# Kernel optimization log

Hardware: AMD Instinct MI355X
Metric: run time of the kernel (lower is better)

The kernel has to match this reference:

```python
import jax, jax.numpy as jnp
import numpy as np

N_FILTER = 64
IMAGE_SIZE = 64
CHANNELS = 3
N_CALLS = 16  # n_calls * 16 with n_calls=1
EPS = 1e-5


def _sobel_kernels(c):
    kx = jnp.array([[-1., 0., 1.], [-2., 0., 2.], [-1., 0., 1.]], jnp.float32) / 8.0
    ky = kx.T
    # depthwise OIHW kernels: (C, 1, 3, 3)
    return jnp.tile(kx[None, None], (c, 1, 1, 1)), jnp.tile(ky[None, None], (c, 1, 1, 1))


def _dwconv(x, k):
    return jax.lax.conv_general_dilated(
        x, k, window_strides=(1, 1), padding='SAME',
        feature_group_count=x.shape[1],
        dimension_numbers=('NCHW', 'OIHW', 'NCHW'))


def setup_inputs() -> dict:
    key = jax.random.key(0)
    k1, k2, k3 = jax.random.split(key, 3)
    B, L = 16, 512
    fin, fout = N_FILTER * 3, N_FILTER
    return {
        'lat': jax.random.normal(k1, (B, L), jnp.float32),
        'Wk': jax.random.normal(k2, (L, fin * fout), jnp.float32) * 0.02,
        'bk': jnp.zeros((fin * fout,), jnp.float32),
        'Wb': jax.random.normal(k3, (L, fout), jnp.float32) * 0.02,
        'bb': jnp.zeros((fout,), jnp.float32),
        'leak_factor': jnp.asarray(0.1, jnp.float32),
    }


def reference(lat, Wk, bk, Wb, bb, leak_factor):
    B = lat.shape[0]
    fin, fout = N_FILTER * 3, N_FILTER
    kx, ky = _sobel_kernels(N_FILTER)

    # seed: zeros with a 1.0 in channel 0 at the image center
    out0 = jnp.zeros((B, N_FILTER, IMAGE_SIZE, IMAGE_SIZE), jnp.float32)
    out0 = out0.at[:, 0, IMAGE_SIZE // 2, IMAGE_SIZE // 2].set(1.0)

    leak = jnp.clip(leak_factor, 0.001, 1000.0)

    # per-sample dynamic 1x1 conv weights/bias (constant across the loop)
    w = (lat @ Wk + bk).reshape(B, fout, fin)   # (B, fout, fin)
    b = (lat @ Wb + bb)                          # (B, fout)

    def step(out, _):
        # Sobel perception: [identity, grad_x, grad_y] -> (B, 3*nf, H, W)
        p = jnp.concatenate([out, _dwconv(out, kx), _dwconv(out, ky)], axis=1)
        # InstanceNorm2d (affine=False): normalize over H, W per sample/channel
        mu = p.mean(axis=(2, 3), keepdims=True)
        var = p.var(axis=(2, 3), keepdims=True)
        p = (p - mu) * jax.lax.rsqrt(var + EPS)
        # latent-conditioned dynamic 1x1 conv
        new = jnp.einsum('bchw,boc->bohw', p, w) + b[:, :, None, None]
        out = out + leak * new
        return out, out

    out, embs = jax.lax.scan(step, out0, None, length=N_CALLS)
    out_embs = jnp.concatenate([out0[None], embs], axis=0)  # (N_CALLS+1, B, nf, H, W)

    out_raw = out[:, :CHANNELS]
    return jnp.clip(out_raw, -1.0, 1.0), out_embs, out_raw
```

## Files before the change

kernel.cpp:

```cpp
#include <hip/hip_runtime.h>
#include <cstdint>
#include <cstddef>

#define NB 16
#define NC 64
#define HW 4096
#define SLICE ((size_t)(NB*NC*HW))
#define NSTEP 16

#define WS_WT    ((size_t)0)
#define WS_BV    ((size_t)196608)
#define WS_LATT  ((size_t)197632)
#define WS_SV    ((size_t)205824)
#define WS_SVMU  ((size_t)208896)

typedef _Float16 half8 __attribute__((ext_vector_type(8)));
typedef float f32x4 __attribute__((ext_vector_type(4)));

__global__ void k_latT(const float* __restrict__ lat, float* __restrict__ latT) {
  int t = threadIdx.x;
  for (int idx = t; idx < 16*512; idx += 256) {
    int b = idx >> 9, k = idx & 511;
    latT[k*16 + b] = lat[idx];
  }
}

__global__ __launch_bounds__(256) void k_w(const float* __restrict__ latT,
    const float* __restrict__ Wk, const float* __restrict__ bk,
    const float* __restrict__ Wb, const float* __restrict__ bb,
    float* __restrict__ wT, float* __restrict__ bvec) {
  int t = threadIdx.x;
  if (blockIdx.x < 48) {
    int j = blockIdx.x*256 + t;
    float acc[16];
#pragma unroll
    for (int b = 0; b < 16; b++) acc[b] = 0.f;
#pragma unroll 4
    for (int k = 0; k < 512; k++) {
      float wv = Wk[(size_t)k*12288 + j];
      const float* lt = (const float*)__builtin_assume_aligned(latT + k*16, 64);
#pragma unroll
      for (int b = 0; b < 16; b++) acc[b] = fmaf(lt[b], wv, acc[b]);
    }
    int o = j / 192, cf = j % 192;
    int g = cf >> 6, c = cf & 63;
    float bkj = bk[j];
#pragma unroll
    for (int b = 0; b < 16; b++)
      wT[(((size_t)(b*3 + g))*64 + o)*64 + c] = acc[b] + bkj;
  } else if (t < 64) {
    int j = t;
    float acc[16];
#pragma unroll
    for (int b = 0; b < 16; b++) acc[b] = 0.f;
    for (int k = 0; k < 512; k++) {
      float wv = Wb[k*64 + j];
      const float* lt = (const float*)__builtin_assume_aligned(latT + k*16, 64);
#pragma unroll
      for (int b = 0; b < 16; b++) acc[b] = fmaf(lt[b], wv, acc[b]);
    }
    float bbj = bb[j];
#pragma unroll
    for (int b = 0; b < 16; b++) bvec[b*64 + j] = acc[b] + bbj;
  }
}

__global__ void k_init(float* __restrict__ e0) {
  int idx4 = (blockIdx.x*256 + threadIdx.x) * 4;
  float4 v = make_float4(0.f, 0.f, 0.f, 0.f);
  if ((idx4 & 262143) == 2080) v.x = 1.0f;
  *(float4*)(e0 + idx4) = v;
}

__global__ __launch_bounds__(256) void k_stats(const float* __restrict__ st,
    float* __restrict__ svb, float* __restrict__ svmub) {
  int c = blockIdx.x, b = blockIdx.y, t = threadIdx.x;
  __shared__ float img[HW];
  __shared__ float red[4][6];
  const size_t chan = (size_t)(b*NC + c) * HW;
  const float4* src4 = (const float4*)(st + chan);
  float4* img4 = (float4*)img;
#pragma unroll
  for (int i = 0; i < 4; i++) img4[i*256 + t] = src4[i*256 + t];
  __syncthreads();
  float s0=0,q0=0,s1=0,q1=0,s2=0,q2=0;
#pragma unroll
  for (int i = 0; i < 4; i++) {
    int base = i*1024 + t*4;
    int h = base >> 6, w0 = base & 63;
#pragma unroll
    for (int jj = 0; jj < 4; jj++) {
      int w = w0 + jj;
      bool wl = (w > 0), wr = (w < 63), hu = (h > 0), hd = (h < 63);
      float a00 = (hu && wl) ? img[(h-1)*64 + (w-1)] : 0.f;
      float a01 =  hu        ? img[(h-1)*64 +  w   ] : 0.f;
      float a02 = (hu && wr) ? img[(h-1)*64 + (w+1)] : 0.f;
      float a10 =  wl        ? img[ h   *64 + (w-1)] : 0.f;
      float a12 =  wr        ? img[ h   *64 + (w+1)] : 0.f;
      float a20 = (hd && wl) ? img[(h+1)*64 + (w-1)] : 0.f;
      float a21 =  hd        ? img[(h+1)*64 +  w   ] : 0.f;
      float a22 = (hd && wr) ? img[(h+1)*64 + (w+1)] : 0.f;
      float v = img[h*64 + w];
      float gx = (a02 - a00 + 2.f*(a12 - a10) + a22 - a20) * 0.125f;
      float gy = (a20 - a00 + 2.f*(a21 - a01) + a22 - a02) * 0.125f;
      s0 += v;  q0 = fmaf(v, v, q0);
      s1 += gx; q1 = fmaf(gx, gx, q1);
      s2 += gy; q2 = fmaf(gy, gy, q2);
    }
  }
#pragma unroll
  for (int off = 32; off >= 1; off >>= 1) {
    s0 += __shfl_xor(s0, off); q0 += __shfl_xor(q0, off);
    s1 += __shfl_xor(s1, off); q1 += __shfl_xor(q1, off);
    s2 += __shfl_xor(s2, off); q2 += __shfl_xor(q2, off);
  }
  int lane = t & 63, wv = t >> 6;
  if (lane == 0) {
    red[wv][0]=s0; red[wv][1]=q0; red[wv][2]=s1;
    red[wv][3]=q1; red[wv][4]=s2; red[wv][5]=q2;
  }
  __syncthreads();
  if (t == 0) {
    float r[6];
#pragma unroll
    for (int u = 0; u < 6; u++) r[u] = red[0][u]+red[1][u]+red[2][u]+red[3][u];
#pragma unroll
    for (int g = 0; g < 3; g++) {
      float mu  = r[2*g] * (1.f/HW);
      float var = fmaxf(r[2*g+1]*(1.f/HW) - mu*mu, 0.f);
      float sv  = 1.f / sqrtf(var + 1e-5f);
      svb  [b*192 + g*64 + c] = sv;
      svmub[b*192 + g*64 + c] = sv * mu;
    }
  }
}

__global__ __launch_bounds__(256, 2) void k_fused(const float* __restrict__ st,
    float* __restrict__ stn, const float* __restrict__ wT,
    const float* __restrict__ bvec, const float* __restrict__ svb,
    const float* __restrict__ svmub, const float* __restrict__ leakp) {
  int r = blockIdx.x, b = blockIdx.y, t = threadIdx.x;
  __shared__ __align__(16) float rawL[32*200];
  __shared__ __align__(16) _Float16 Bhi[4*192*8];
  __shared__ __align__(16) _Float16 Blo[4*192*8];
  __shared__ __align__(16) _Float16 Whi[3*64*32];
  __shared__ __align__(16) _Float16 Wlo[3*64*32];
  __shared__ float svL[192], svmuL[192], biasL[192], bvecL[64];

  if (t < 192) { svL[t] = svb[b*192 + t]; svmuL[t] = svmub[b*192 + t]; }
  if (t < 64) bvecL[t] = bvec[b*64 + t];
  float leak = fminf(fmaxf(leakp[0], 0.001f), 1000.f);

  int lane = t & 63;
  int wt = t >> 6;
  const float* stb = st + (size_t)b*NC*HW;
  float biasacc = 0.f;
  f32x4 accA[4] = {}; f32x4 accB[12] = {}; f32x4 accC[12] = {};

  for (int kc = 0; kc < 2; kc++) {
    __syncthreads();
#pragma unroll
    for (int i = 0; i < 6; i++) {
      int u = t + i*256;
      int c_rel = u / 48, q = u % 48;
      int rho = q >> 4, quad = q & 15;
      int row = r - 1 + rho;
      float4 v = make_float4(0.f,0.f,0.f,0.f);
      if (row >= 0 && row < 64)
        v = *(const float4*)(stb + (size_t)(kc*32 + c_rel)*HW + row*64 + quad*4);
      *(float4*)(rawL + c_rel*200 + rho*64 + quad*4) = v;
    }
    if (t < 192) {
      int g = t >> 6, o = t & 63;
      const float* wrow = wT + (((size_t)(b*3 + g))*64 + o)*64 + kc*32;
#pragma unroll
      for (int s = 0; s < 4; s++) {
        float4 va = *(const float4*)(wrow + s*8);
        float4 vb = *(const float4*)(wrow + s*8 + 4);
        float wv[8] = {va.x,va.y,va.z,va.w,vb.x,vb.y,vb.z,vb.w};
        half8 hv, lv;
#pragma unroll
        for (int jj = 0; jj < 8; jj++) {
          int cg = g*64 + kc*32 + s*8 + jj;
          float scaled = wv[jj] * svL[cg];
          biasacc = fmaf(wv[jj], svmuL[cg], biasacc);
          _Float16 h = (_Float16)scaled;
          hv[jj] = h;
          lv[jj] = (_Float16)(scaled - (float)h);
        }
        int sidx = (g*64 + o)*32 + ((s ^ (o & 3)) << 3);
        *(half8*)(Whi + sidx) = hv;
        *(half8*)(Wlo + sidx) = lv;
      }
    }
    __syncthreads();
#pragma unroll
    for (int i = 0; i < 3; i++) {
      int v = t + i*256;
      int c8 = v / 192, px = v % 192;
      half8 hv, lv;
#pragma unroll
      for (int ii = 0; ii < 8; ii++) {
        float x = rawL[(c8*8 + ii)*200 + px];
        _Float16 h = (_Float16)x;
        hv[ii] = h;
        lv[ii] = (_Float16)(x - (float)h);
      }
      *(half8*)(Bhi + (c8*192 + px)*8) = hv;
      *(half8*)(Blo + (c8*192 + px)*8) = lv;
    }
    __syncthreads();
    half8 ahi[3], alo[3];
#pragma unroll
    for (int g = 0; g < 3; g++) {
      int oa = wt*16 + (lane & 15);
      int sidx = (g*64 + oa)*32 + (((lane >> 4) ^ (oa & 3)) << 3);
      ahi[g] = *(const half8*)(Whi + sidx);
      alo[g] = *(const half8*)(Wlo + sidx);
    }
#pragma unroll
    for (int n = 0; n < 12; n++) {
      int bidx = ((lane >> 4)*192 + n*16 + (lane & 15))*8;
      half8 bh = *(const half8*)(Bhi + bidx);
      half8 bl = *(const half8*)(Blo + bidx);
      accB[n] = __builtin_amdgcn_mfma_f32_16x16x32_f16(ahi[1], bh, accB[n], 0,0,0);
      accB[n] = __builtin_amdgcn_mfma_f32_16x16x32_f16(ahi[1], bl, accB[n], 0,0,0);
      accB[n] = __builtin_amdgcn_mfma_f32_16x16x32_f16(alo[1], bh, accB[n], 0,0,0);
      accC[n] = __builtin_amdgcn_mfma_f32_16x16x32_f16(ahi[2], bh, accC[n], 0,0,0);
      accC[n] = __builtin_amdgcn_mfma_f32_16x16x32_f16(ahi[2], bl, accC[n], 0,0,0);
      accC[n] = __builtin_amdgcn_mfma_f32_16x16x32_f16(alo[2], bh, accC[n], 0,0,0);
      if (n >= 4 && n < 8) {
        accA[n-4] = __builtin_amdgcn_mfma_f32_16x16x32_f16(ahi[0], bh, accA[n-4], 0,0,0);
        accA[n-4] = __builtin_amdgcn_mfma_f32_16x16x32_f16(ahi[0], bl, accA[n-4], 0,0,0);
        accA[n-4] = __builtin_amdgcn_mfma_f32_16x16x32_f16(alo[0], bh, accA[n-4], 0,0,0);
      }
    }
  }

  if (t < 192) biasL[t] = biasacc;
  __syncthreads();

#pragma unroll
  for (int j = 0; j < 4; j++) {
    int o = wt*16 + ((lane >> 4) << 2) + j;
    float Sx[4], Sy[4];
#pragma unroll
    for (int nc = 0; nc < 4; nc++) {
      Sx[nc] = accB[nc][j] + 2.f*accB[4+nc][j] + accB[8+nc][j];
      Sy[nc] = accC[8+nc][j] - accC[nc][j];
    }
    float bt = bvecL[o] - biasL[o] - biasL[64+o] - biasL[128+o];
#pragma unroll
    for (int nc = 0; nc < 4; nc++) {
      int nm = (nc > 0) ? nc-1 : 0;
      int np = (nc < 3) ? nc+1 : 3;
      float xl1 = __shfl(Sx[nc], (lane - 1) & 63);
      float xl2 = (nc > 0) ? __shfl(Sx[nm], (lane + 15) & 63) : 0.f;
      float xL  = (lane & 15) ? xl1 : xl2;
      float xr1 = __shfl(Sx[nc], (lane + 1) & 63);
      float xr2 = (nc < 3) ? __shfl(Sx[np], (lane - 15) & 63) : 0.f;
      float xR  = ((lane & 15) == 15) ? xr2 : xr1;
      float yl1 = __shfl(Sy[nc], (lane - 1) & 63);
      float yl2 = (nc > 0) ? __shfl(Sy[nm], (lane + 15) & 63) : 0.f;
      float yL  = (lane & 15) ? yl1 : yl2;
      float yr1 = __shfl(Sy[nc], (lane + 1) & 63);
      float yr2 = (nc < 3) ? __shfl(Sy[np], (lane - 15) & 63) : 0.f;
      float yR  = ((lane & 15) == 15) ? yr2 : yr1;
      float gx = (xR - xL) * 0.125f;
      float gy = (yL + 2.f*Sy[nc] + yR) * 0.125f;
      float nw = accA[nc][j] + gx + gy + bt;
      int w = nc*16 + (lane & 15);
      size_t gi = (size_t)(b*NC + o)*HW + (size_t)r*64 + w;
      stn[gi] = st[gi] + leak * nw;
    }
  }
}

__global__ void k_final(const float* __restrict__ stF, float* __restrict__ out0,
                        float* __restrict__ out2) {
  int i4 = (blockIdx.x*256 + threadIdx.x)*4;
  int b = i4 / 12288, rr = i4 % 12288;
  float4 v = *(const float4*)(stF + (size_t)b*(NC*HW) + rr);
  float4 cv;
  cv.x = fminf(fmaxf(v.x,-1.f),1.f);
  cv.y = fminf(fmaxf(v.y,-1.f),1.f);
  cv.z = fminf(fmaxf(v.z,-1.f),1.f);
  cv.w = fminf(fmaxf(v.w,-1.f),1.f);
  *(float4*)(out0 + i4) = cv;
  *(float4*)(out2 + i4) = v;
}

extern "C" void kernel_launch(void* const* d_in, const int* in_sizes, int n_in,
                              void* d_out, int out_size, void* d_ws, size_t ws_size,
                              hipStream_t stream) {
  const float* lat   = (const float*)d_in[0];
  const float* Wk    = (const float*)d_in[1];
  const float* bk    = (const float*)d_in[2];
  const float* Wb    = (const float*)d_in[3];
  const float* bb    = (const float*)d_in[4];
  const float* leakp = (const float*)d_in[5];
  float* out = (float*)d_out;
  float* ws  = (float*)d_ws;
  float* wT    = ws + WS_WT;
  float* bvec  = ws + WS_BV;
  float* latT  = ws + WS_LATT;
  float* svbuf = ws + WS_SV;
  float* svmub = ws + WS_SVMU;
  float* out0 = out;
  float* embs = out + 196608;
  float* out2 = out + 196608 + 17*SLICE;

  hipLaunchKernelGGL(k_latT, dim3(1),    dim3(256), 0, stream, lat, latT);
  hipLaunchKernelGGL(k_w,    dim3(49),   dim3(256), 0, stream, latT, Wk, bk, Wb, bb, wT, bvec);
  hipLaunchKernelGGL(k_init, dim3(4096), dim3(256), 0, stream, embs);
  for (int tstep = 0; tstep < NSTEP; tstep++) {
    const float* stc = embs + (size_t)tstep*SLICE;
    float*       stn = embs + (size_t)(tstep+1)*SLICE;
    hipLaunchKernelGGL(k_stats, dim3(64,16), dim3(256), 0, stream, stc, svbuf, svmub);
    hipLaunchKernelGGL(k_fused, dim3(64,16), dim3(256), 0, stream,
                       stc, stn, wT, bvec, svbuf, svmub, leakp);
  }
  hipLaunchKernelGGL(k_final, dim3(192), dim3(256), 0, stream,
                     embs + (size_t)NSTEP*SLICE, out0, out2);
}
```

Before: 730.2 us.

## Pipeline k_fused channel chunks, swizzle LDS, slide stats window, fold final kernel

```diff
diff --git a/kernel.cpp b/kernel.cpp
--- a/kernel.cpp
+++ b/kernel.cpp
@@ -83,30 +83,45 @@
 #pragma unroll
   for (int i = 0; i < 4; i++) img4[i*256 + t] = src4[i*256 + t];
   __syncthreads();
+
+  int w = t & 63;
+  int h0 = (t >> 6) * 16;
+  bool wl = (w > 0), wr = (w < 63);
   float s0=0,q0=0,s1=0,q1=0,s2=0,q2=0;
-#pragma unroll
-  for (int i = 0; i < 4; i++) {
-    int base = i*1024 + t*4;
-    int h = base >> 6, w0 = base & 63;
-#pragma unroll
-    for (int jj = 0; jj < 4; jj++) {
-      int w = w0 + jj;
-      bool wl = (w > 0), wr = (w < 63), hu = (h > 0), hd = (h < 63);
-      float a00 = (hu && wl) ? img[(h-1)*64 + (w-1)] : 0.f;
-      float a01 =  hu        ? img[(h-1)*64 +  w   ] : 0.f;
-      float a02 = (hu && wr) ? img[(h-1)*64 + (w+1)] : 0.f;
-      float a10 =  wl        ? img[ h   *64 + (w-1)] : 0.f;
-      float a12 =  wr        ? img[ h   *64 + (w+1)] : 0.f;
-      float a20 = (hd && wl) ? img[(h+1)*64 + (w-1)] : 0.f;
-      float a21 =  hd        ? img[(h+1)*64 +  w   ] : 0.f;
-      float a22 = (hd && wr) ? img[(h+1)*64 + (w+1)] : 0.f;
-      float v = img[h*64 + w];
-      float gx = (a02 - a00 + 2.f*(a12 - a10) + a22 - a20) * 0.125f;
-      float gy = (a20 - a00 + 2.f*(a21 - a01) + a22 - a02) * 0.125f;
-      s0 += v;  q0 = fmaf(v, v, q0);
-      s1 += gx; q1 = fmaf(gx, gx, q1);
-      s2 += gy; q2 = fmaf(gy, gy, q2);
-    }
+  float d_prev=0.f, s_prev=0.f, d_cur, s_cur, v_cur;
+  if (h0 > 0) {
+    const float* row = img + (h0-1)*64;
+    float xl = wl ? row[w-1] : 0.f;
+    float xc = row[w];
+    float xr = wr ? row[w+1] : 0.f;
+    d_prev = xr - xl; s_prev = xl + 2.f*xc + xr;
+  }
+  {
+    const float* row = img + h0*64;
+    float xl = wl ? row[w-1] : 0.f;
+    float xc = row[w];
+    float xr = wr ? row[w+1] : 0.f;
+    d_cur = xr - xl; s_cur = xl + 2.f*xc + xr; v_cur = xc;
+  }
+#pragma unroll
+  for (int k = 0; k < 16; k++) {
+    int hn = h0 + k + 1;
+    float d_nxt=0.f, s_nxt=0.f, v_nxt=0.f;
+    if (hn < 64) {
+      const float* row = img + hn*64;
+      float xl = wl ? row[w-1] : 0.f;
+      float xc = row[w];
+      float xr = wr ? row[w+1] : 0.f;
+      d_nxt = xr - xl; s_nxt = xl + 2.f*xc + xr; v_nxt = xc;
+    }
+    float gx = (d_prev + 2.f*d_cur + d_nxt) * 0.125f;
+    float gy = (s_nxt - s_prev) * 0.125f;
+    float v = v_cur;
+    s0 += v;  q0 = fmaf(v, v, q0);
+    s1 += gx; q1 = fmaf(gx, gx, q1);
+    s2 += gy; q2 = fmaf(gy, gy, q2);
+    d_prev = d_cur; s_prev = s_cur;
+    d_cur = d_nxt; s_cur = s_nxt; v_cur = v_nxt;
   }
 #pragma unroll
   for (int off = 32; off >= 1; off >>= 1) {
@@ -135,109 +150,141 @@
   }
 }
 
+struct SB {
+  alignas(16) _Float16 Bhi[6144];
+  alignas(16) _Float16 Blo[6144];
+  alignas(16) _Float16 Whi[6144];
+  alignas(16) _Float16 Wlo[6144];
+  float svL[192], svmuL[192], biasL[192], bvecL[64];
+};
+
 __global__ __launch_bounds__(256, 2) void k_fused(const float* __restrict__ st,
     float* __restrict__ stn, const float* __restrict__ wT,
     const float* __restrict__ bvec, const float* __restrict__ svb,
-    const float* __restrict__ svmub, const float* __restrict__ leakp) {
-  int r = blockIdx.x, b = blockIdx.y, t = threadIdx.x;
-  __shared__ __align__(16) float rawL[32*200];
-  __shared__ __align__(16) _Float16 Bhi[4*192*8];
-  __shared__ __align__(16) _Float16 Blo[4*192*8];
-  __shared__ __align__(16) _Float16 Whi[3*64*32];
-  __shared__ __align__(16) _Float16 Wlo[3*64*32];
-  __shared__ float svL[192], svmuL[192], biasL[192], bvecL[64];
-
-  if (t < 192) { svL[t] = svb[b*192 + t]; svmuL[t] = svmub[b*192 + t]; }
-  if (t < 64) bvecL[t] = bvec[b*64 + t];
+    const float* __restrict__ svmub, const float* __restrict__ leakp,
+    float* __restrict__ out0, float* __restrict__ out2, int last) {
+  __shared__ SB sh;
+  int bid = blockIdx.x, t = threadIdx.x;
+  int b = bid >> 6;
+  int r = (bid & 7) * 8 + ((bid >> 3) & 7);
+  int lane = t & 63, wt = t >> 6;
+  const float* stb = st + (size_t)b*NC*HW;
   float leak = fminf(fmaxf(leakp[0], 0.001f), 1000.f);
 
-  int lane = t & 63;
-  int wt = t >> 6;
-  const float* stb = st + (size_t)b*NC*HW;
+  if (t < 192) { sh.svL[t] = svb[b*192 + t]; sh.svmuL[t] = svmub[b*192 + t]; }
+  if (t < 64) sh.bvecL[t] = bvec[b*64 + t];
+
   float biasacc = 0.f;
   f32x4 accA[4] = {}; f32x4 accB[12] = {}; f32x4 accC[12] = {};
-
-  for (int kc = 0; kc < 2; kc++) {
-    __syncthreads();
-#pragma unroll
-    for (int i = 0; i < 6; i++) {
-      int u = t + i*256;
-      int c_rel = u / 48, q = u % 48;
-      int rho = q >> 4, quad = q & 15;
-      int row = r - 1 + rho;
-      float4 v = make_float4(0.f,0.f,0.f,0.f);
-      if (row >= 0 && row < 64)
-        v = *(const float4*)(stb + (size_t)(kc*32 + c_rel)*HW + row*64 + quad*4);
-      *(float4*)(rawL + c_rel*200 + rho*64 + quad*4) = v;
-    }
-    if (t < 192) {
-      int g = t >> 6, o = t & 63;
-      const float* wrow = wT + (((size_t)(b*3 + g))*64 + o)*64 + kc*32;
-#pragma unroll
-      for (int s = 0; s < 4; s++) {
-        float4 va = *(const float4*)(wrow + s*8);
-        float4 vb = *(const float4*)(wrow + s*8 + 4);
-        float wv[8] = {va.x,va.y,va.z,va.w,vb.x,vb.y,vb.z,vb.w};
-        half8 hv, lv;
-#pragma unroll
-        for (int jj = 0; jj < 8; jj++) {
-          int cg = g*64 + kc*32 + s*8 + jj;
-          float scaled = wv[jj] * svL[cg];
-          biasacc = fmaf(wv[jj], svmuL[cg], biasacc);
-          _Float16 h = (_Float16)scaled;
-          hv[jj] = h;
-          lv[jj] = (_Float16)(scaled - (float)h);
-        }
-        int sidx = (g*64 + o)*32 + ((s ^ (o & 3)) << 3);
-        *(half8*)(Whi + sidx) = hv;
-        *(half8*)(Wlo + sidx) = lv;
-      }
-    }
-    __syncthreads();
-#pragma unroll
-    for (int i = 0; i < 3; i++) {
-      int v = t + i*256;
-      int c8 = v / 192, px = v % 192;
-      half8 hv, lv;
-#pragma unroll
-      for (int ii = 0; ii < 8; ii++) {
-        float x = rawL[(c8*8 + ii)*200 + px];
-        _Float16 h = (_Float16)x;
-        hv[ii] = h;
-        lv[ii] = (_Float16)(x - (float)h);
-      }
-      *(half8*)(Bhi + (c8*192 + px)*8) = hv;
-      *(half8*)(Blo + (c8*192 + px)*8) = lv;
-    }
-    __syncthreads();
-    half8 ahi[3], alo[3];
-#pragma unroll
-    for (int g = 0; g < 3; g++) {
-      int oa = wt*16 + (lane & 15);
-      int sidx = (g*64 + oa)*32 + (((lane >> 4) ^ (oa & 3)) << 3);
-      ahi[g] = *(const half8*)(Whi + sidx);
-      alo[g] = *(const half8*)(Wlo + sidx);
-    }
-#pragma unroll
-    for (int n = 0; n < 12; n++) {
-      int bidx = ((lane >> 4)*192 + n*16 + (lane & 15))*8;
-      half8 bh = *(const half8*)(Bhi + bidx);
-      half8 bl = *(const half8*)(Blo + bidx);
-      accB[n] = __builtin_amdgcn_mfma_f32_16x16x32_f16(ahi[1], bh, accB[n], 0,0,0);
-      accB[n] = __builtin_amdgcn_mfma_f32_16x16x32_f16(ahi[1], bl, accB[n], 0,0,0);
-      accB[n] = __builtin_amdgcn_mfma_f32_16x16x32_f16(alo[1], bh, accB[n], 0,0,0);
-      accC[n] = __builtin_amdgcn_mfma_f32_16x16x32_f16(ahi[2], bh, accC[n], 0,0,0);
-      accC[n] = __builtin_amdgcn_mfma_f32_16x16x32_f16(ahi[2], bl, accC[n], 0,0,0);
-      accC[n] = __builtin_amdgcn_mfma_f32_16x16x32_f16(alo[2], bh, accC[n], 0,0,0);
-      if (n >= 4 && n < 8) {
-        accA[n-4] = __builtin_amdgcn_mfma_f32_16x16x32_f16(ahi[0], bh, accA[n-4], 0,0,0);
-        accA[n-4] = __builtin_amdgcn_mfma_f32_16x16x32_f16(ahi[0], bl, accA[n-4], 0,0,0);
-        accA[n-4] = __builtin_amdgcn_mfma_f32_16x16x32_f16(alo[0], bh, accA[n-4], 0,0,0);
-      }
-    }
-  }
-
-  if (t < 192) biasL[t] = biasacc;
+  float xw0[3][8], xw1[3][8];
+
+#define LOADW(KC, XW)                                                    \
+  _Pragma("unroll")                                                      \
+  for (int i = 0; i < 3; i++) {                                          \
+    int u = t + i*256;                                                   \
+    int c8 = u / 192, pxu = u % 192;                                     \
+    int rho = pxu >> 6, ww = pxu & 63;                                   \
+    int row = r - 1 + rho;                                               \
+    bool ok = (row >= 0) && (row < 64);                                  \
+    int rowc = ok ? row : 0;                                             \
+    const float* gp = stb + (size_t)((KC)*32 + c8*8)*HW + rowc*64 + ww;  \
+    _Pragma("unroll")                                                    \
+    for (int ii = 0; ii < 8; ii++) {                                     \
+      float val = gp[(size_t)ii*HW];                                     \
+      XW[i][ii] = ok ? val : 0.f;                                        \
+    }                                                                    \
+  }
+
+#define PACKW(XW)                                                        \
+  _Pragma("unroll")                                                      \
+  for (int i = 0; i < 3; i++) {                                          \
+    int u = t + i*256;                                                   \
+    int c8 = u / 192, pxu = u % 192;                                     \
+    half8 hv, lv;                                                        \
+    _Pragma("unroll")                                                    \
+    for (int ii = 0; ii < 8; ii++) {                                     \
+      float x = XW[i][ii];                                               \
+      _Float16 h = (_Float16)x;                                          \
+      hv[ii] = h;                                                        \
+      lv[ii] = (_Float16)(x - (float)h);                                 \
+    }                                                                    \
+    int di = (c8*192 + (pxu ^ c8)) * 8;                                  \
+    *(half8*)(sh.Bhi + di) = hv;                                         \
+    *(half8*)(sh.Blo + di) = lv;                                         \
+  }
+
+#define WSTAGE(KC)                                                       \
+  if (t < 192) {                                                         \
+    int g = t >> 6, o = t & 63;                                          \
+    const float* wrow = wT + (((size_t)(b*3 + g))*64 + o)*64 + (KC)*32;  \
+    _Pragma("unroll")                                                    \
+    for (int s = 0; s < 4; s++) {                                        \
+      float4 va = *(const float4*)(wrow + s*8);                          \
+      float4 vb4 = *(const float4*)(wrow + s*8 + 4);                     \
+      float wv[8] = {va.x,va.y,va.z,va.w,vb4.x,vb4.y,vb4.z,vb4.w};       \
+      half8 hv, lv;                                                      \
+      _Pragma("unroll")                                                  \
+      for (int jj = 0; jj < 8; jj++) {                                   \
+        int cg = g*64 + (KC)*32 + s*8 + jj;                              \
+        float scaled = wv[jj] * sh.svL[cg];                              \
+        biasacc = fmaf(wv[jj], sh.svmuL[cg], biasacc);                   \
+        _Float16 h = (_Float16)scaled;                                   \
+        hv[jj] = h;                                                      \
+        lv[jj] = (_Float16)(scaled - (float)h);                          \
+      }                                                                  \
+      int swz = (s ^ (o & 3) ^ ((o >> 2) & 3)) & 3;                      \
+      int sidx = (g*64 + o)*32 + (swz << 3);                             \
+      *(half8*)(sh.Whi + sidx) = hv;                                     \
+      *(half8*)(sh.Wlo + sidx) = lv;                                     \
+    }                                                                    \
+  }
+
+#define MFMAS()                                                          \
+  {                                                                      \
+    half8 ahi[3], alo[3];                                                \
+    int oa = wt*16 + (lane & 15);                                        \
+    int c4 = lane >> 4;                                                  \
+    int slotx = (c4 ^ (oa & 3) ^ ((oa >> 2) & 3)) & 3;                   \
+    _Pragma("unroll")                                                    \
+    for (int g = 0; g < 3; g++) {                                        \
+      int sidx = (g*64 + oa)*32 + (slotx << 3);                          \
+      ahi[g] = *(const half8*)(sh.Whi + sidx);                           \
+      alo[g] = *(const half8*)(sh.Wlo + sidx);                           \
+    }                                                                    \
+    _Pragma("unroll")                                                    \
+    for (int n = 0; n < 12; n++) {                                       \
+      int px = n*16 + (lane & 15);                                       \
+      int bidx = (c4*192 + (px ^ c4))*8;                                 \
+      half8 bh = *(const half8*)(sh.Bhi + bidx);                         \
+      half8 bl = *(const half8*)(sh.Blo + bidx);                         \
+      accB[n] = __builtin_amdgcn_mfma_f32_16x16x32_f16(ahi[1], bh, accB[n], 0,0,0); \
+      accB[n] = __builtin_amdgcn_mfma_f32_16x16x32_f16(ahi[1], bl, accB[n], 0,0,0); \
+      accB[n] = __builtin_amdgcn_mfma_f32_16x16x32_f16(alo[1], bh, accB[n], 0,0,0); \
+      accC[n] = __builtin_amdgcn_mfma_f32_16x16x32_f16(ahi[2], bh, accC[n], 0,0,0); \
+      accC[n] = __builtin_amdgcn_mfma_f32_16x16x32_f16(ahi[2], bl, accC[n], 0,0,0); \
+      accC[n] = __builtin_amdgcn_mfma_f32_16x16x32_f16(alo[2], bh, accC[n], 0,0,0); \
+      if (n >= 4 && n < 8) {                                             \
+        accA[n-4] = __builtin_amdgcn_mfma_f32_16x16x32_f16(ahi[0], bh, accA[n-4], 0,0,0); \
+        accA[n-4] = __builtin_amdgcn_mfma_f32_16x16x32_f16(ahi[0], bl, accA[n-4], 0,0,0); \
+        accA[n-4] = __builtin_amdgcn_mfma_f32_16x16x32_f16(alo[0], bh, accA[n-4], 0,0,0); \
+      }                                                                  \
+    }                                                                    \
+  }
+
+  LOADW(0, xw0)
+  __syncthreads();
+  PACKW(xw0)
+  WSTAGE(0)
+  __syncthreads();
+  LOADW(1, xw1)
+  MFMAS()
+  __syncthreads();
+  PACKW(xw1)
+  WSTAGE(1)
+  __syncthreads();
+  MFMAS()
+
+  if (t < 192) sh.biasL[t] = biasacc;
   __syncthreads();
 
 #pragma unroll
@@ -249,7 +296,7 @@
       Sx[nc] = accB[nc][j] + 2.f*accB[4+nc][j] + accB[8+nc][j];
       Sy[nc] = accC[8+nc][j] - accC[nc][j];
     }
-    float bt = bvecL[o] - biasL[o] - biasL[64+o] - biasL[128+o];
+    float bt = sh.bvecL[o] - sh.biasL[o] - sh.biasL[64+o] - sh.biasL[128+o];
 #pragma unroll
     for (int nc = 0; nc < 4; nc++) {
       int nm = (nc > 0) ? nc-1 : 0;
@@ -269,25 +316,21 @@
       float gx = (xR - xL) * 0.125f;
       float gy = (yL + 2.f*Sy[nc] + yR) * 0.125f;
       float nw = accA[nc][j] + gx + gy + bt;
-      int w = nc*16 + (lane & 15);
-      size_t gi = (size_t)(b*NC + o)*HW + (size_t)r*64 + w;
-      stn[gi] = st[gi] + leak * nw;
-    }
-  }
-}
-
-__global__ void k_final(const float* __restrict__ stF, float* __restrict__ out0,
-                        float* __restrict__ out2) {
-  int i4 = (blockIdx.x*256 + threadIdx.x)*4;
-  int b = i4 / 12288, rr = i4 % 12288;
-  float4 v = *(const float4*)(stF + (size_t)b*(NC*HW) + rr);
-  float4 cv;
-  cv.x = fminf(fmaxf(v.x,-1.f),1.f);
-  cv.y = fminf(fmaxf(v.y,-1.f),1.f);
-  cv.z = fminf(fmaxf(v.z,-1.f),1.f);
-  cv.w = fminf(fmaxf(v.w,-1.f),1.f);
-  *(float4*)(out0 + i4) = cv;
-  *(float4*)(out2 + i4) = v;
+      int wpx = nc*16 + (lane & 15);
+      size_t gi = (size_t)(b*NC + o)*HW + (size_t)r*64 + wpx;
+      float nv = st[gi] + leak * nw;
+      stn[gi] = nv;
+      if (last && o < 3) {
+        size_t oi = (size_t)(b*3 + o)*HW + (size_t)r*64 + wpx;
+        out2[oi] = nv;
+        out0[oi] = fminf(fmaxf(nv, -1.f), 1.f);
+      }
+    }
+  }
+#undef LOADW
+#undef PACKW
+#undef WSTAGE
+#undef MFMAS
 }
 
 extern "C" void kernel_launch(void* const* d_in, const int* in_sizes, int n_in,
@@ -317,9 +360,8 @@
     const float* stc = embs + (size_t)tstep*SLICE;
     float*       stn = embs + (size_t)(tstep+1)*SLICE;
     hipLaunchKernelGGL(k_stats, dim3(64,16), dim3(256), 0, stream, stc, svbuf, svmub);
-    hipLaunchKernelGGL(k_fused, dim3(64,16), dim3(256), 0, stream,
-                       stc, stn, wT, bvec, svbuf, svmub, leakp);
-  }
-  hipLaunchKernelGGL(k_final, dim3(192), dim3(256), 0, stream,
-                     embs + (size_t)NSTEP*SLICE, out0, out2);
-}
+    hipLaunchKernelGGL(k_fused, dim3(1024), dim3(256), 0, stream,
+                       stc, stn, wT, bvec, svbuf, svmub, leakp,
+                       out0, out2, (int)(tstep == NSTEP-1));
+  }
+}
```

New measurement: 599.9 us. 17.9% less time.

## Precompute fp16 hi/lo state planes, two rows per block, fuse final output

Applied to the files above, without the earlier changes.

```diff
diff --git a/kernel.cpp b/kernel.cpp
--- a/kernel.cpp
+++ b/kernel.cpp
@@ -10,22 +10,15 @@
 
 #define WS_WT    ((size_t)0)
 #define WS_BV    ((size_t)196608)
-#define WS_LATT  ((size_t)197632)
-#define WS_SV    ((size_t)205824)
-#define WS_SVMU  ((size_t)208896)
+#define WS_SV    ((size_t)197632)
+#define WS_SVMU  ((size_t)200704)
+#define WS_PLA   ((size_t)203776)
+#define WS_PLB   ((size_t)4398080)
 
 typedef _Float16 half8 __attribute__((ext_vector_type(8)));
 typedef float f32x4 __attribute__((ext_vector_type(4)));
 
-__global__ void k_latT(const float* __restrict__ lat, float* __restrict__ latT) {
-  int t = threadIdx.x;
-  for (int idx = t; idx < 16*512; idx += 256) {
-    int b = idx >> 9, k = idx & 511;
-    latT[k*16 + b] = lat[idx];
-  }
-}
-
-__global__ __launch_bounds__(256) void k_w(const float* __restrict__ latT,
+__global__ __launch_bounds__(256) void k_w(const float* __restrict__ lat,
     const float* __restrict__ Wk, const float* __restrict__ bk,
     const float* __restrict__ Wb, const float* __restrict__ bb,
     float* __restrict__ wT, float* __restrict__ bvec) {
@@ -38,9 +31,8 @@
 #pragma unroll 4
     for (int k = 0; k < 512; k++) {
       float wv = Wk[(size_t)k*12288 + j];
-      const float* lt = (const float*)__builtin_assume_aligned(latT + k*16, 64);
-#pragma unroll
-      for (int b = 0; b < 16; b++) acc[b] = fmaf(lt[b], wv, acc[b]);
+#pragma unroll
+      for (int b = 0; b < 16; b++) acc[b] = fmaf(lat[b*512 + k], wv, acc[b]);
     }
     int o = j / 192, cf = j % 192;
     int g = cf >> 6, c = cf & 63;
@@ -55,9 +47,8 @@
     for (int b = 0; b < 16; b++) acc[b] = 0.f;
     for (int k = 0; k < 512; k++) {
       float wv = Wb[k*64 + j];
-      const float* lt = (const float*)__builtin_assume_aligned(latT + k*16, 64);
-#pragma unroll
-      for (int b = 0; b < 16; b++) acc[b] = fmaf(lt[b], wv, acc[b]);
+#pragma unroll
+      for (int b = 0; b < 16; b++) acc[b] = fmaf(lat[b*512 + k], wv, acc[b]);
     }
     float bbj = bb[j];
 #pragma unroll
@@ -65,48 +56,50 @@
   }
 }
 
-__global__ void k_init(float* __restrict__ e0) {
-  int idx4 = (blockIdx.x*256 + threadIdx.x) * 4;
+__global__ void k_init(float* __restrict__ e0, float* __restrict__ plA) {
+  int f4 = blockIdx.x*256 + threadIdx.x;
   float4 v = make_float4(0.f, 0.f, 0.f, 0.f);
-  if ((idx4 & 262143) == 2080) v.x = 1.0f;
-  *(float4*)(e0 + idx4) = v;
+  if (f4 < 1048576) {
+    if ((f4 & 65535) == 520) v.x = 1.0f;
+    *(float4*)(e0 + (size_t)f4*4) = v;
+  } else {
+    int g4 = f4 - 1048576;
+    if ((g4 & 65535) == 2080)
+      v.x = __uint_as_float(0x00003C00u);
+    *(float4*)(plA + (size_t)g4*4) = v;
+  }
 }
 
 __global__ __launch_bounds__(256) void k_stats(const float* __restrict__ st,
     float* __restrict__ svb, float* __restrict__ svmub) {
   int c = blockIdx.x, b = blockIdx.y, t = threadIdx.x;
-  __shared__ float img[HW];
   __shared__ float red[4][6];
-  const size_t chan = (size_t)(b*NC + c) * HW;
-  const float4* src4 = (const float4*)(st + chan);
-  float4* img4 = (float4*)img;
-#pragma unroll
-  for (int i = 0; i < 4; i++) img4[i*256 + t] = src4[i*256 + t];
-  __syncthreads();
+  const float* base = st + (size_t)(b*NC + c) * HW;
+  int w = t & 63, wv = t >> 6, h0 = wv * 16;
+  float x[18];
+#pragma unroll
+  for (int i = 0; i < 18; i++) {
+    int row = h0 - 1 + i;
+    x[i] = (row >= 0 && row < 64) ? base[row*64 + w] : 0.f;
+  }
+  float d[18], s[18];
+#pragma unroll
+  for (int i = 0; i < 18; i++) {
+    float xl = __shfl(x[i], (w + 63) & 63);
+    float xr = __shfl(x[i], (w + 1) & 63);
+    if (w == 0)  xl = 0.f;
+    if (w == 63) xr = 0.f;
+    d[i] = xr - xl; s[i] = xl + 2.f*x[i] + xr;
+  }
   float s0=0,q0=0,s1=0,q1=0,s2=0,q2=0;
 #pragma unroll
-  for (int i = 0; i < 4; i++) {
-    int base = i*1024 + t*4;
-    int h = base >> 6, w0 = base & 63;
-#pragma unroll
-    for (int jj = 0; jj < 4; jj++) {
-      int w = w0 + jj;
-      bool wl = (w > 0), wr = (w < 63), hu = (h > 0), hd = (h < 63);
-      float a00 = (hu && wl) ? img[(h-1)*64 + (w-1)] : 0.f;
-      float a01 =  hu        ? img[(h-1)*64 +  w   ] : 0.f;
-      float a02 = (hu && wr) ? img[(h-1)*64 + (w+1)] : 0.f;
-      float a10 =  wl        ? img[ h   *64 + (w-1)] : 0.f;
-      float a12 =  wr        ? img[ h   *64 + (w+1)] : 0.f;
-      float a20 = (hd && wl) ? img[(h+1)*64 + (w-1)] : 0.f;
-      float a21 =  hd        ? img[(h+1)*64 +  w   ] : 0.f;
-      float a22 = (hd && wr) ? img[(h+1)*64 + (w+1)] : 0.f;
-      float v = img[h*64 + w];
-      float gx = (a02 - a00 + 2.f*(a12 - a10) + a22 - a20) * 0.125f;
-      float gy = (a20 - a00 + 2.f*(a21 - a01) + a22 - a02) * 0.125f;
-      s0 += v;  q0 = fmaf(v, v, q0);
-      s1 += gx; q1 = fmaf(gx, gx, q1);
-      s2 += gy; q2 = fmaf(gy, gy, q2);
-    }
+  for (int k = 0; k < 16; k++) {
+    float v  = x[k+1];
+    float gx = (d[k] + 2.f*d[k+1] + d[k+2]) * 0.125f;
+    float gy = (s[k+2] - s[k]) * 0.125f;
+    s0 += v;  q0 = fmaf(v, v, q0);
+    s1 += gx; q1 = fmaf(gx, gx, q1);
+    s2 += gy; q2 = fmaf(gy, gy, q2);
   }
 #pragma unroll
   for (int off = 32; off >= 1; off >>= 1) {
@@ -114,7 +107,7 @@
     s1 += __shfl_xor(s1, off); q1 += __shfl_xor(q1, off);
     s2 += __shfl_xor(s2, off); q2 += __shfl_xor(q2, off);
   }
-  int lane = t & 63, wv = t >> 6;
+  int lane = t & 63;
   if (lane == 0) {
     red[wv][0]=s0; red[wv][1]=q0; red[wv][2]=s1;
     red[wv][3]=q1; red[wv][4]=s2; red[wv][5]=q2;
@@ -135,159 +128,170 @@
   }
 }
 
-__global__ __launch_bounds__(256, 2) void k_fused(const float* __restrict__ st,
+struct SG {
+  alignas(16) _Float16 Bwin[32768];
+  float biasL[64];
+};
+
+__global__ __launch_bounds__(256, 2) void k_gemm(const float* __restrict__ st,
     float* __restrict__ stn, const float* __restrict__ wT,
     const float* __restrict__ bvec, const float* __restrict__ svb,
-    const float* __restrict__ svmub, const float* __restrict__ leakp) {
-  int r = blockIdx.x, b = blockIdx.y, t = threadIdx.x;
-  __shared__ __align__(16) float rawL[32*200];
-  __shared__ __align__(16) _Float16 Bhi[4*192*8];
-  __shared__ __align__(16) _Float16 Blo[4*192*8];
-  __shared__ __align__(16) _Float16 Whi[3*64*32];
-  __shared__ __align__(16) _Float16 Wlo[3*64*32];
-  __shared__ float svL[192], svmuL[192], biasL[192], bvecL[64];
-
-  if (t < 192) { svL[t] = svb[b*192 + t]; svmuL[t] = svmub[b*192 + t]; }
-  if (t < 64) bvecL[t] = bvec[b*64 + t];
+    const float* __restrict__ svmub, const _Float16* __restrict__ plR,
+    _Float16* __restrict__ plW, const float* __restrict__ leakp,
+    float* __restrict__ out0, float* __restrict__ out2, int last) {
+  __shared__ SG sh;
+  int bid = blockIdx.x, t = threadIdx.x;
+  int b = bid >> 5;
+  int r0 = ((((bid & 7) << 2) | ((bid >> 3) & 3))) << 1;
+  int lane = t & 63, wt = t >> 6, c4 = lane >> 4;
   float leak = fminf(fmaxf(leakp[0], 0.001f), 1000.f);
 
-  int lane = t & 63;
-  int wt = t >> 6;
-  const float* stb = st + (size_t)b*NC*HW;
+  const _Float16* plb = plR + (size_t)b*524288;
+#pragma unroll
+  for (int i = 0; i < 16; i++) {
+    int u = t + i*256;
+    int pl = u >> 11, rest = u & 2047;
+    int pxg = (r0 - 1)*64 + (rest & 255);
+    int pxc = pxg < 0 ? 0 : (pxg > 4095 ? 4095 : pxg);
+    const _Float16* gp = plb + ((size_t)pl*8 + (rest >> 8))*32768 + (size_t)pxc*8;
+    float4 v = *(const float4*)gp;
+    if (pxg < 0 || pxg > 4095) v = make_float4(0.f,0.f,0.f,0.f);
+    *(float4*)(sh.Bwin + (size_t)u*8) = v;
+  }
+
+  int oa = wt*16 + (lane & 15);
+  half8 whi[3][2], wlo[3][2];
   float biasacc = 0.f;
-  f32x4 accA[4] = {}; f32x4 accB[12] = {}; f32x4 accC[12] = {};
-
-  for (int kc = 0; kc < 2; kc++) {
-    __syncthreads();
-#pragma unroll
-    for (int i = 0; i < 6; i++) {
-      int u = t + i*256;
-      int c_rel = u / 48, q = u % 48;
-      int rho = q >> 4, quad = q & 15;
-      int row = r - 1 + rho;
-      float4 v = make_float4(0.f,0.f,0.f,0.f);
-      if (row >= 0 && row < 64)
-        v = *(const float4*)(stb + (size_t)(kc*32 + c_rel)*HW + row*64 + quad*4);
-      *(float4*)(rawL + c_rel*200 + rho*64 + quad*4) = v;
-    }
-    if (t < 192) {
-      int g = t >> 6, o = t & 63;
-      const float* wrow = wT + (((size_t)(b*3 + g))*64 + o)*64 + kc*32;
-#pragma unroll
-      for (int s = 0; s < 4; s++) {
-        float4 va = *(const float4*)(wrow + s*8);
-        float4 vb = *(const float4*)(wrow + s*8 + 4);
-        float wv[8] = {va.x,va.y,va.z,va.w,vb.x,vb.y,vb.z,vb.w};
-        half8 hv, lv;
-#pragma unroll
-        for (int jj = 0; jj < 8; jj++) {
-          int cg = g*64 + kc*32 + s*8 + jj;
-          float scaled = wv[jj] * svL[cg];
-          biasacc = fmaf(wv[jj], svmuL[cg], biasacc);
-          _Float16 h = (_Float16)scaled;
-          hv[jj] = h;
-          lv[jj] = (_Float16)(scaled - (float)h);
+#pragma unroll
+  for (int g = 0; g < 3; g++) {
+#pragma unroll
+    for (int kc = 0; kc < 2; kc++) {
+      const float* wrow = wT + (((size_t)(b*3 + g))*64 + oa)*64 + kc*32 + c4*8;
+      const float* svp  = svb   + b*192 + g*64 + kc*32 + c4*8;
+      const float* svmp = svmub + b*192 + g*64 + kc*32 + c4*8;
+      float4 wa = *(const float4*)wrow;  float4 wb2 = *(const float4*)(wrow + 4);
+      float4 sa = *(const float4*)svp;   float4 sb2 = *(const float4*)(svp + 4);
+      float4 ma = *(const float4*)svmp;  float4 mb2 = *(const float4*)(svmp + 4);
+      float wv[8] = {wa.x,wa.y,wa.z,wa.w, wb2.x,wb2.y,wb2.z,wb2.w};
+      float sv[8] = {sa.x,sa.y,sa.z,sa.w, sb2.x,sb2.y,sb2.z,sb2.w};
+      float mv[8] = {ma.x,ma.y,ma.z,ma.w, mb2.x,mb2.y,mb2.z,mb2.w};
+      half8 hv, lv;
+#pragma unroll
+      for (int jj = 0; jj < 8; jj++) {
+        float scaled = wv[jj] * sv[jj];
+        biasacc = fmaf(wv[jj], mv[jj], biasacc);
+        _Float16 h = (_Float16)scaled;
+        hv[jj] = h;
+        lv[jj] = (_Float16)(scaled - (float)h);
+      }
+      whi[g][kc] = hv; wlo[g][kc] = lv;
+    }
+  }
+  biasacc += __shfl_xor(biasacc, 16);
+  biasacc += __shfl_xor(biasacc, 32);
+  if (c4 == 0) sh.biasL[oa] = bvec[b*64 + oa] - biasacc;
+  __syncthreads();
+
+#pragma unroll
+  for (int rr = 0; rr < 2; rr++) {
+    int r = r0 + rr;
+    f32x4 accA[4] = {}; f32x4 accB[12] = {}; f32x4 accC[12] = {};
+#pragma unroll
+    for (int kc = 0; kc < 2; kc++) {
+#pragma unroll
+      for (int n = 0; n < 12; n++) {
+        int pxl = rr*64 + n*16 + (lane & 15);
+        half8 bh = *(const half8*)(sh.Bwin + ((size_t)(     kc*4 + c4)*256 + pxl)*8);
+        half8 bl = *(const half8*)(sh.Bwin + ((size_t)(8 +  kc*4 + c4)*256 + pxl)*8);
+        accB[n] = __builtin_amdgcn_mfma_f32_16x16x32_f16(whi[1][kc], bh, accB[n], 0,0,0);
+        accB[n] = __builtin_amdgcn_mfma_f32_16x16x32_f16(whi[1][kc], bl, accB[n], 0,0,0);
+        accB[n] = __builtin_amdgcn_mfma_f32_16x16x32_f16(wlo[1][kc], bh, accB[n], 0,0,0);
+        accC[n] = __builtin_amdgcn_mfma_f32_16x16x32_f16(whi[2][kc], bh, accC[n], 0,0,0);
+        accC[n] = __builtin_amdgcn_mfma_f32_16x16x32_f16(whi[2][kc], bl, accC[n], 0,0,0);
+        accC[n] = __builtin_amdgcn_mfma_f32_16x16x32_f16(wlo[2][kc], bh, accC[n], 0,0,0);
+        if (n >= 4 && n < 8) {
+          accA[n-4] = __builtin_amdgcn_mfma_f32_16x16x32_f16(whi[0][kc], bh, accA[n-4], 0,0,0);
+          accA[n-4] = __builtin_amdgcn_mfma_f32_16x16x32_f16(whi[0][kc], bl, accA[n-4], 0,0,0);
+          accA[n-4] = __builtin_amdgcn_mfma_f32_16x16x32_f16(wlo[0][kc], bh, accA[n-4], 0,0,0);
         }
-        int sidx = (g*64 + o)*32 + ((s ^ (o & 3)) << 3);
-        *(half8*)(Whi + sidx) = hv;
-        *(half8*)(Wlo + sidx) = lv;
-      }
-    }
-    __syncthreads();
-#pragma unroll
-    for (int i = 0; i < 3; i++) {
-      int v = t + i*256;
-      int c8 = v / 192, px = v % 192;
-      half8 hv, lv;
-#pragma unroll
-      for (int ii = 0; ii < 8; ii++) {
-        float x = rawL[(c8*8 + ii)*200 + px];
-        _Float16 h = (_Float16)x;
-        hv[ii] = h;
-        lv[ii] = (_Float16)(x - (float)h);
-      }
-      *(half8*)(Bhi + (c8*192 + px)*8) = hv;
-      *(half8*)(Blo + (c8*192 + px)*8) = lv;
-    }
-    __syncthreads();
-    half8 ahi[3], alo[3];
-#pragma unroll
-    for (int g = 0; g < 3; g++) {
-      int oa = wt*16 + (lane & 15);
-      int sidx = (g*64 + oa)*32 + (((lane >> 4) ^ (oa & 3)) << 3);
-      ahi[g] = *(const half8*)(Whi + sidx);
-      alo[g] = *(const half8*)(Wlo + sidx);
-    }
-#pragma unroll
-    for (int n = 0; n < 12; n++) {
-      int bidx = ((lane >> 4)*192 + n*16 + (lane & 15))*8;
-      half8 bh = *(const half8*)(Bhi + bidx);
-      half8 bl = *(const half8*)(Blo + bidx);
-      accB[n] = __builtin_amdgcn_mfma_f32_16x16x32_f16(ahi[1], bh, accB[n], 0,0,0);
-      accB[n] = __builtin_amdgcn_mfma_f32_16x16x32_f16(ahi[1], bl, accB[n], 0,0,0);
-      accB[n] = __builtin_amdgcn_mfma_f32_16x16x32_f16(alo[1], bh, accB[n], 0,0,0);
-      accC[n] = __builtin_amdgcn_mfma_f32_16x16x32_f16(ahi[2], bh, accC[n], 0,0,0);
-      accC[n] = __builtin_amdgcn_mfma_f32_16x16x32_f16(ahi[2], bl, accC[n], 0,0,0);
-      accC[n] = __builtin_amdgcn_mfma_f32_16x16x32_f16(alo[2], bh, accC[n], 0,0,0);
-      if (n >= 4 && n < 8) {
-        accA[n-4] = __builtin_amdgcn_mfma_f32_16x16x32_f16(ahi[0], bh, accA[n-4], 0,0,0);
-        accA[n-4] = __builtin_amdgcn_mfma_f32_16x16x32_f16(ahi[0], bl, accA[n-4], 0,0,0);
-        accA[n-4] = __builtin_amdgcn_mfma_f32_16x16x32_f16(alo[0], bh, accA[n-4], 0,0,0);
-      }
-    }
-  }
-
-  if (t < 192) biasL[t] = biasacc;
-  __syncthreads();
-
-#pragma unroll
-  for (int j = 0; j < 4; j++) {
-    int o = wt*16 + ((lane >> 4) << 2) + j;
-    float Sx[4], Sy[4];
-#pragma unroll
-    for (int nc = 0; nc < 4; nc++) {
-      Sx[nc] = accB[nc][j] + 2.f*accB[4+nc][j] + accB[8+nc][j];
-      Sy[nc] = accC[8+nc][j] - accC[nc][j];
-    }
-    float bt = bvecL[o] - biasL[o] - biasL[64+o] - biasL[128+o];
-#pragma unroll
-    for (int nc = 0; nc < 4; nc++) {
-      int nm = (nc > 0) ? nc-1 : 0;
-      int np = (nc < 3) ? nc+1 : 3;
-      float xl1 = __shfl(Sx[nc], (lane - 1) & 63);
-      float xl2 = (nc > 0) ? __shfl(Sx[nm], (lane + 15) & 63) : 0.f;
-      float xL  = (lane & 15) ? xl1 : xl2;
-      float xr1 = __shfl(Sx[nc], (lane + 1) & 63);
-      float xr2 = (nc < 3) ? __shfl(Sx[np], (lane - 15) & 63) : 0.f;
-      float xR  = ((lane & 15) == 15) ? xr2 : xr1;
-      float yl1 = __shfl(Sy[nc], (lane - 1) & 63);
-      float yl2 = (nc > 0) ? __shfl(Sy[nm], (lane + 15) & 63) : 0.f;
-      float yL  = (lane & 15) ? yl1 : yl2;
-      float yr1 = __shfl(Sy[nc], (lane + 1) & 63);
-      float yr2 = (nc < 3) ? __shfl(Sy[np], (lane - 15) & 63) : 0.f;
-      float yR  = ((lane & 15) == 15) ? yr2 : yr1;
-      float gx = (xR - xL) * 0.125f;
-      float gy = (yL + 2.f*Sy[nc] + yR) * 0.125f;
-      float nw = accA[nc][j] + gx + gy + bt;
-      int w = nc*16 + (lane & 15);
-      size_t gi = (size_t)(b*NC + o)*HW + (size_t)r*64 + w;
-      stn[gi] = st[gi] + leak * nw;
-    }
-  }
-}
-
-__global__ void k_final(const float* __restrict__ stF, float* __restrict__ out0,
-                        float* __restrict__ out2) {
-  int i4 = (blockIdx.x*256 + threadIdx.x)*4;
-  int b = i4 / 12288, rr = i4 % 12288;
-  float4 v = *(const float4*)(stF + (size_t)b*(NC*HW) + rr);
-  float4 cv;
-  cv.x = fminf(fmaxf(v.x,-1.f),1.f);
-  cv.y = fminf(fmaxf(v.y,-1.f),1.f);
-  cv.z = fminf(fmaxf(v.z,-1.f),1.f);
-  cv.w = fminf(fmaxf(v.w,-1.f),1.f);
-  *(float4*)(out0 + i4) = cv;
-  *(float4*)(out2 + i4) = v;
+      }
+    }
+
+    float nv16[16];
+#pragma unroll
+    for (int j = 0; j < 4; j++) {
+      int o = wt*16 + (c4 << 2) + j;
+      float Sx[4], Sy[4];
+#pragma unroll
+      for (int nc = 0; nc < 4; nc++) {
+        Sx[nc] = accB[nc][j] + 2.f*accB[4+nc][j] + accB[8+nc][j];
+        Sy[nc] = accC[8+nc][j] - accC[nc][j];
+      }
+      float bt = sh.biasL[o];
+#pragma unroll
+      for (int nc = 0; nc < 4; nc++) {
+        int nm = (nc > 0) ? nc-1 : 0;
+        int np = (nc < 3) ? nc+1 : 3;
+        float xl1 = __shfl(Sx[nc], (lane - 1) & 63);
+        float xl2 = (nc > 0) ? __shfl(Sx[nm], (lane + 15) & 63) : 0.f;
+        float xL  = (lane & 15) ? xl1 : xl2;
+        float xr1 = __shfl(Sx[nc], (lane + 1) & 63);
+        float xr2 = (nc < 3) ? __shfl(Sx[np], (lane - 15) & 63) : 0.f;
+        float xR  = ((lane & 15) == 15) ? xr2 : xr1;
+        float yl1 = __shfl(Sy[nc], (lane - 1) & 63);
+        float yl2 = (nc > 0) ? __shfl(Sy[nm], (lane + 15) & 63) : 0.f;
+        float yL  = (lane & 15) ? yl1 : yl2;
+        float yr1 = __shfl(Sy[nc], (lane + 1) & 63);
+        float yr2 = (nc < 3) ? __shfl(Sy[np], (lane - 15) & 63) : 0.f;
+        float yR  = ((lane & 15) == 15) ? yr2 : yr1;
+        float gx = (xR - xL) * 0.125f;
+        float gy = (yL + 2.f*Sy[nc] + yR) * 0.125f;
+        float nw = accA[nc][j] + gx + gy + bt;
+        int wpx = nc*16 + (lane & 15);
+        size_t gi = (size_t)(b*NC + o)*HW + (size_t)r*64 + wpx;
+        float nvv = st[gi] + leak * nw;
+        stn[gi] = nvv;
+        nv16[j*4 + nc] = nvv;
+        if (last && o < 3) {
+          size_t oi = (size_t)(b*3 + o)*HW + (size_t)r*64 + wpx;
+          out2[oi] = nvv;
+          out0[oi] = fminf(fmaxf(nvv, -1.f), 1.f);
+        }
+      }
+    }
+
+    if (!last) {
+      int pl = c4 & 1;
+      int g8 = wt*2 + (c4 >> 1);
+      _Float16* pw = plW + (size_t)b*524288 + ((size_t)pl*8 + g8)*32768;
+#pragma unroll
+      for (int nc = 0; nc < 4; nc++) {
+        float own[4], rcv[4];
+#pragma unroll
+        for (int j = 0; j < 4; j++) {
+          own[j] = nv16[j*4 + nc];
+          rcv[j] = __shfl_xor(own[j], 16);
+        }
+        float xx[8];
+#pragma unroll
+        for (int jj = 0; jj < 8; jj++)
+          xx[jj] = ((jj >> 2) == (c4 & 1)) ? own[jj & 3] : rcv[jj & 3];
+        half8 v8;
+        if (pl == 0) {
+#pragma unroll
+          for (int jj = 0; jj < 8; jj++) v8[jj] = (_Float16)xx[jj];
+        } else {
+#pragma unroll
+          for (int jj = 0; jj < 8; jj++) {
+            _Float16 h = (_Float16)xx[jj];
+            v8[jj] = (_Float16)(xx[jj] - (float)h);
+          }
+        }
+        int gpx = r*64 + nc*16 + (lane & 15);
+        *(half8*)(pw + (size_t)gpx*8) = v8;
+      }
+    }
+  }
 }
 
 extern "C" void kernel_launch(void* const* d_in, const int* in_sizes, int n_in,
@@ -303,23 +307,22 @@
   float* ws  = (float*)d_ws;
   float* wT    = ws + WS_WT;
   float* bvec  = ws + WS_BV;
-  float* latT  = ws + WS_LATT;
   float* svbuf = ws + WS_SV;
   float* svmub = ws + WS_SVMU;
+  _Float16* plbuf[2] = { (_Float16*)(ws + WS_PLA), (_Float16*)(ws + WS_PLB) };
   float* out0 = out;
   float* embs = out + 196608;
   float* out2 = out + 196608 + 17*SLICE;
 
-  hipLaunchKernelGGL(k_latT, dim3(1),    dim3(256), 0, stream, lat, latT);
-  hipLaunchKernelGGL(k_w,    dim3(49),   dim3(256), 0, stream, latT, Wk, bk, Wb, bb, wT, bvec);
-  hipLaunchKernelGGL(k_init, dim3(4096), dim3(256), 0, stream, embs);
+  hipLaunchKernelGGL(k_w,    dim3(49),   dim3(256), 0, stream, lat, Wk, bk, Wb, bb, wT, bvec);
+  hipLaunchKernelGGL(k_init, dim3(8192), dim3(256), 0, stream, embs, ws + WS_PLA);
   for (int tstep = 0; tstep < NSTEP; tstep++) {
     const float* stc = embs + (size_t)tstep*SLICE;
     float*       stn = embs + (size_t)(tstep+1)*SLICE;
     hipLaunchKernelGGL(k_stats, dim3(64,16), dim3(256), 0, stream, stc, svbuf, svmub);
-    hipLaunchKernelGGL(k_fused, dim3(64,16), dim3(256), 0, stream,
-                       stc, stn, wT, bvec, svbuf, svmub, leakp);
-  }
-  hipLaunchKernelGGL(k_final, dim3(192), dim3(256), 0, stream,
-                     embs + (size_t)NSTEP*SLICE, out0, out2);
-}
+    hipLaunchKernelGGL(k_gemm, dim3(512), dim3(256), 0, stream,
+                       stc, stn, wT, bvec, svbuf, svmub,
+                       plbuf[tstep & 1], plbuf[(tstep+1) & 1], leakp,
+                       out0, out2, (int)(tstep == NSTEP-1));
+  }
+}
```

New measurement: 600.4 us. 1.22x faster.
